# Performance work log

Hardware: AMD Instinct MI355X
Metric: run time of the kernel (lower is better)

## Reference

```python
import jax, jax.numpy as jnp
import numpy as np


def setup_inputs() -> dict:
    key = jax.random.key(0)
    k1, k2, k3 = jax.random.split(key, 3)
    inp = jax.random.normal(k1, (32, 128, 56, 56), dtype=jnp.float32)
    # kaiming-style scale for a 3x3 conv kernel
    fan_in = 128 * 3 * 3
    kernel = jax.random.normal(k2, (256, 128, 3, 3), dtype=jnp.float32) * np.float32(np.sqrt(2.0 / fan_in))
    bias = jax.random.normal(k3, (256,), dtype=jnp.float32)
    return {"inp": inp, "kernel": kernel, "bias": bias}


def reference(inp, kernel, bias):
    # 3x3 conv, stride 1, padding 1 (SAME), NCHW / OIHW layout, plus bias.
    out = jax.lax.conv_general_dilated(
        inp, kernel,
        window_strides=(1, 1),
        padding=((1, 1), (1, 1)),
        dimension_numbers=("NCHW", "OIHW", "NCHW"),
    )
    return out + bias[None, :, None, None]
```

## Files before the change

### kernel.cpp

```cpp
#include <hip/hip_runtime.h>
#include <hip/hip_bf16.h>


#define C_IN   128
#define K_OUT  256
#define HW     56
#define IMG    3136
#define NBATCH 32
#define PW     58
#define IN_WS_USHORT ((size_t)4*NBATCH*PW*256*8)
#define WT_WS_USHORT ((size_t)12*2*1536*8)

typedef __bf16 bf16x8 __attribute__((ext_vector_type(8)));
typedef float  f32x4  __attribute__((ext_vector_type(4)));
typedef unsigned short ushort8 __attribute__((ext_vector_type(8)));

__device__ inline unsigned short f2bf(float f) {
    unsigned int u = __builtin_bit_cast(unsigned int, f);
    u += ((u >> 16) & 1u) + 0x7FFFu;
    return (unsigned short)(u >> 16);
}

__device__ __forceinline__ void gl2lds16(const unsigned short* g, unsigned short* l) {
    __builtin_amdgcn_global_load_lds(
        (const __attribute__((address_space(1))) unsigned int*)g,
        (__attribute__((address_space(3))) unsigned int*)l, 16, 0, 0);
}

__global__ void prep_input(const float* __restrict__ inp,
                           unsigned short* __restrict__ dst) {
    __shared__ unsigned short tile[C_IN * 57];
    int n = blockIdx.x / PW, py = blockIdx.x % PW;
    ushort8* d8 = (ushort8*)dst;
    const bool border = (py == 0 || py == PW - 1);
    if (!border) {
        const float* src = inp + (size_t)n * C_IN * IMG + (py - 1) * HW;
        for (int i = threadIdx.x; i < C_IN * HW; i += 256) {
            int c = i / HW, x = i - c * HW;
            tile[c * 57 + x] = f2bf(src[c * IMG + x]);
        }
        __syncthreads();
    }
    for (int i = threadIdx.x; i < 1024; i += 256) {
        int cq = i >> 8, rem = i & 255;
        int X = ((rem >> 6) & 3) * 16 + (rem & 15);
        int cc = (rem >> 4) & 3;
        ushort8 v = (ushort8)0;
        if (!border && X >= 1 && X <= HW) {
#pragma unroll
            for (int e = 0; e < 8; ++e)
                v[e] = tile[(cq * 32 + cc * 8 + e) * 57 + (X - 1)];
        }
        d8[((size_t)(cq * NBATCH + n) * PW + py) * 256 + rem] = v;
    }
}

__global__ void prep_weights(const float* __restrict__ w,
                             unsigned short* __restrict__ dst) {
    int chunk = blockIdx.x * 256 + threadIdx.x;
    int p = chunk / 3072, rem = chunk - p * 3072;
    int koh = rem / 1536, rem2 = rem - koh * 1536;
    int s = rem2 / 512, rem3 = rem2 - s * 512;
    int koq = rem3 >> 6, cc = (rem3 >> 4) & 3, kor = rem3 & 15;
    int ko = koh * 128 + koq * 16 + kor;
    int cq = p / 3, r = p - 3 * cq;
    ushort8 v;
#pragma unroll
    for (int e = 0; e < 8; ++e)
        v[e] = f2bf(w[(ko * C_IN + cq * 32 + cc * 8 + e) * 9 + r * 3 + s]);
    ((ushort8*)dst)[chunk] = v;
}

__global__ __launch_bounds__(256, 2) void conv_mfma(
        const unsigned short* __restrict__ In,
        const unsigned short* __restrict__ Wt,
        const float* __restrict__ bias,
        float* __restrict__ out) {
    __shared__ unsigned short smem[16384];

    const int tid = threadIdx.x;
    const int lane = tid & 63, wv = tid >> 6;
    const int l15 = lane & 15, lk = lane >> 4;
    const int koh = blockIdx.y;
    const int by = blockIdx.x;
    const int n = by / 14, rb = (by % 14) * 4;

    const int wkol = (wv & 1) * 64;
    const int wpx  = (wv >> 1) * 112;
    const int wlane = (wv & 1) * 2048 + lk * 128 + l15 * 8;

    int yl[7], xp[3][7];
#pragma unroll
    for (int nf = 0; nf < 7; ++nf) {
        int p = wpx + nf * 16 + l15;
        yl[nf] = p / 56;
        int x = p - yl[nf] * 56;
#pragma unroll
        for (int s = 0; s < 3; ++s) {
            int X = x + s;
            xp[s][nf] = ((X >> 4) << 10) + lk * 256 + ((X & 15) << 4);
        }
    }

    f32x4 acc[4][7];
#pragma unroll
    for (int m = 0; m < 4; ++m)
#pragma unroll
        for (int nf = 0; nf < 7; ++nf) acc[m][nf] = (f32x4)0.0f;

    bf16x8 wbuf[2][4];

#define LOAD_WS(G_) do {                                                    \
    if constexpr ((G_) <= 35) {                                             \
        constexpr int p_ = (G_) / 3, sx_ = (G_) % 3;                        \
        const unsigned short* wp = Wt + ((size_t)(p_ * 2 + koh)) * 12288    \
                                   + sx_ * 4096 + wlane;                    \
        _Pragma("unroll")                                                   \
        for (int m = 0; m < 4; ++m)                                         \
            wbuf[(G_) & 1][m] = *(const bf16x8*)(wp + m * 512);             \
    } } while (0)

#define STAGE_ROW(C_, T_) do {                                              \
    gl2lds16(In + ((size_t)(((C_) * NBATCH + n) * PW + rb + (T_))) * 2048 + tid * 8, \
             &smem[((6 * (C_) + (T_)) & 7) * 2048 + tid * 8]);              \
} while (0)

#define STEP(PH, S_) do {                                                   \
    constexpr int g_ = (PH) * 3 + (S_);                                     \
    LOAD_WS(g_ + 1);                                                        \
    { const char* ib = (const char*)smem;                                   \
      bf16x8 b[7];                                                          \
      _Pragma("unroll")                                                     \
      for (int nf = 0; nf < 7; ++nf)                                        \
          b[nf] = *(const bf16x8*)(ib + roff[nf] + xp[(S_)][nf]);           \
      __builtin_amdgcn_s_setprio(1);                                        \
      _Pragma("unroll")                                                     \
      for (int m = 0; m < 4; ++m)                                           \
          _Pragma("unroll")                                                 \
          for (int nf = 0; nf < 7; ++nf)                                    \
              acc[m][nf] = __builtin_amdgcn_mfma_f32_16x16x32_bf16(         \
                  wbuf[g_ & 1][m], b[nf], acc[m][nf], 0, 0, 0);             \
      __builtin_amdgcn_s_setprio(0);                                        \
    }                                                                       \
} while (0)

    STAGE_ROW(0, 0); STAGE_ROW(0, 1); STAGE_ROW(0, 2); STAGE_ROW(0, 3);
    asm volatile("" ::: "memory");
    LOAD_WS(0);

#define PHASE(PH) do {                                                      \
    constexpr int cqp_ = (PH) / 3, rp_ = (PH) % 3;                          \
    asm volatile("s_waitcnt vmcnt(4)" ::: "memory");                        \
    asm volatile("s_barrier" ::: "memory");                                 \
    if constexpr (rp_ == 0) {                                               \
        STAGE_ROW(cqp_, 4);                                                 \
        if constexpr (cqp_ < 3) STAGE_ROW(cqp_ + 1, 0);                     \
    } else if constexpr (rp_ == 1) {                                        \
        STAGE_ROW(cqp_, 5);                                                 \
        if constexpr (cqp_ < 3) STAGE_ROW(cqp_ + 1, 1);                     \
    } else {                                                                \
        if constexpr (cqp_ < 3) { STAGE_ROW(cqp_ + 1, 2); STAGE_ROW(cqp_ + 1, 3); } \
    }                                                                       \
    { int roff[7];                                                          \
      _Pragma("unroll")                                                     \
      for (int nf = 0; nf < 7; ++nf)                                        \
          roff[nf] = ((6 * cqp_ + rp_ + yl[nf]) & 7) << 12;                 \
      STEP(PH, 0); STEP(PH, 1); STEP(PH, 2);                                \
    }                                                                       \
} while (0)

    PHASE(0);  PHASE(1);  PHASE(2);  PHASE(3);
    PHASE(4);  PHASE(5);  PHASE(6);  PHASE(7);
    PHASE(8);  PHASE(9);  PHASE(10); PHASE(11);

#undef PHASE
#undef STEP
#undef STAGE_ROW
#undef LOAD_WS

    const int sp0 = rb * 56 + wpx;
#pragma unroll
    for (int m = 0; m < 4; ++m) {
        int kb = koh * 128 + wkol + m * 16 + lk * 4;
        f32x4 bs = *(const f32x4*)(bias + kb);
#pragma unroll
        for (int nf = 0; nf < 7; ++nf) {
            float* ob = out + ((size_t)(n * K_OUT + kb) * IMG) + sp0 + nf * 16 + l15;
#pragma unroll
            for (int j = 0; j < 4; ++j)
                ob[(size_t)j * IMG] = acc[m][nf][j] + bs[j];
        }
    }
}

__global__ void conv_naive(const float* __restrict__ inp,
                           const float* __restrict__ ker,
                           const float* __restrict__ bias,
                           float* __restrict__ out, int total) {
    int o = blockIdx.x * blockDim.x + threadIdx.x;
    if (o >= total) return;
    int x = o % HW, y = (o / HW) % HW, ko = (o / IMG) % K_OUT, n = o / (IMG * K_OUT);
    float acc = bias[ko];
    for (int c = 0; c < C_IN; ++c)
        for (int r = 0; r < 3; ++r) {
            int iy = y + r - 1; if ((unsigned)iy >= HW) continue;
            for (int s = 0; s < 3; ++s) {
                int ix = x + s - 1; if ((unsigned)ix >= HW) continue;
                acc += inp[((n * C_IN + c) * HW + iy) * HW + ix]
                     * ker[((ko * C_IN + c) * 3 + r) * 3 + s];
            }
        }
    out[o] = acc;
}

extern "C" void kernel_launch(void* const* d_in, const int* in_sizes, int n_in,
                              void* d_out, int out_size, void* d_ws, size_t ws_size,
                              hipStream_t stream) {
    const float* inp  = (const float*)d_in[0];
    const float* ker  = (const float*)d_in[1];
    const float* bias = (const float*)d_in[2];
    float* out = (float*)d_out;

    const size_t need = (IN_WS_USHORT + WT_WS_USHORT) * 2;
    if (ws_size < need) {
        int total = NBATCH * K_OUT * IMG;
        conv_naive<<<(total + 255) / 256, 256, 0, stream>>>(inp, ker, bias, out, total);
        return;
    }

    unsigned short* inb = (unsigned short*)d_ws;
    unsigned short* wtb = inb + IN_WS_USHORT;

    prep_input<<<NBATCH * PW, 256, 0, stream>>>(inp, inb);
    prep_weights<<<144, 256, 0, stream>>>(ker, wtb);

    conv_mfma<<<dim3(448, 2), 256, 0, stream>>>(inb, wtb, bias, out);
}
```

Baseline: 98.69 us.

## Replace 8-row LDS ring with double-buffered 6-row tiles per channel quarter

Input staging changes from a rolling 8-row LDS ring, refilled two rows per phase across 12 phases, to a double buffer holding 6 rows for each of the 4 channel quarters. Each phase prefetches the whole next quarter and then runs all 9 filter taps. This cuts the s_waitcnt plus barrier synchronisation points from 12 to 4 and simplifies the row-offset arithmetic, since the modulo-8 wrap is gone. In exchange, LDS use per block grows from 32 KB to 48 KB, which could limit occupancy, and prefetches are issued in larger, coarser batches.

```diff
diff --git a/kernel.cpp b/kernel.cpp
--- a/kernel.cpp
+++ b/kernel.cpp
@@ -76,7 +76,7 @@
         const unsigned short* __restrict__ Wt,
         const float* __restrict__ bias,
         float* __restrict__ out) {
-    __shared__ unsigned short smem[16384];
+    __shared__ unsigned short smem[24576];
 
     const int tid = threadIdx.x;
     const int lane = tid & 63, wv = tid >> 6;
@@ -120,16 +120,18 @@
             wbuf[(G_) & 1][m] = *(const bf16x8*)(wp + m * 512);             \
     } } while (0)
 
-#define STAGE_ROW(C_, T_) do {                                              \
-    gl2lds16(In + ((size_t)(((C_) * NBATCH + n) * PW + rb + (T_))) * 2048 + tid * 8, \
-             &smem[((6 * (C_) + (T_)) & 7) * 2048 + tid * 8]);              \
-} while (0)
-
-#define STEP(PH, S_) do {                                                   \
-    constexpr int g_ = (PH) * 3 + (S_);                                     \
+#define STAGE6(CQN) do {                                                    \
+    _Pragma("unroll")                                                       \
+    for (int t = 0; t < 6; ++t)                                             \
+        gl2lds16(In + ((size_t)(((CQN) * NBATCH + n) * PW + rb + t)) * 2048 + tid * 8, \
+                 &smem[(((CQN) & 1) * 6 + t) * 2048 + tid * 8]);            \
+    asm volatile("" ::: "memory");    \
+} while (0)
+
+#define STEP(CQ_, R_, S_) do {                                              \
+    constexpr int g_ = (CQ_) * 9 + (R_) * 3 + (S_);                         \
     LOAD_WS(g_ + 1);                                                        \
-    { const char* ib = (const char*)smem;                                   \
-      bf16x8 b[7];                                                          \
+    { bf16x8 b[7];                                                          \
       _Pragma("unroll")                                                     \
       for (int nf = 0; nf < 7; ++nf)                                        \
           b[nf] = *(const bf16x8*)(ib + roff[nf] + xp[(S_)][nf]);           \
@@ -144,38 +146,33 @@
     }                                                                       \
 } while (0)
 
-    STAGE_ROW(0, 0); STAGE_ROW(0, 1); STAGE_ROW(0, 2); STAGE_ROW(0, 3);
-    asm volatile("" ::: "memory");
+#define ROFF(CQ_, R_) do {                                                  \
+    _Pragma("unroll")                                                       \
+    for (int nf = 0; nf < 7; ++nf)                                          \
+        roff[nf] = (((CQ_) & 1) * 6 + (R_) + yl[nf]) << 12;                 \
+} while (0)
+
+    STAGE6(0);
     LOAD_WS(0);
 
-#define PHASE(PH) do {                                                      \
-    constexpr int cqp_ = (PH) / 3, rp_ = (PH) % 3;                          \
+#define PHASE(CQ_) do {                                                     \
     asm volatile("s_waitcnt vmcnt(4)" ::: "memory");                        \
     asm volatile("s_barrier" ::: "memory");                                 \
-    if constexpr (rp_ == 0) {                                               \
-        STAGE_ROW(cqp_, 4);                                                 \
-        if constexpr (cqp_ < 3) STAGE_ROW(cqp_ + 1, 0);                     \
-    } else if constexpr (rp_ == 1) {                                        \
-        STAGE_ROW(cqp_, 5);                                                 \
-        if constexpr (cqp_ < 3) STAGE_ROW(cqp_ + 1, 1);                     \
-    } else {                                                                \
-        if constexpr (cqp_ < 3) { STAGE_ROW(cqp_ + 1, 2); STAGE_ROW(cqp_ + 1, 3); } \
+    if constexpr ((CQ_) < 3) STAGE6((CQ_) + 1);                             \
+    { const char* ib = (const char*)smem;                                   \
+      int roff[7];                                                          \
+      ROFF(CQ_, 0); STEP(CQ_,0,0); STEP(CQ_,0,1); STEP(CQ_,0,2);            \
+      ROFF(CQ_, 1); STEP(CQ_,1,0); STEP(CQ_,1,1); STEP(CQ_,1,2);            \
+      ROFF(CQ_, 2); STEP(CQ_,2,0); STEP(CQ_,2,1); STEP(CQ_,2,2);            \
     }                                                                       \
-    { int roff[7];                                                          \
-      _Pragma("unroll")                                                     \
-      for (int nf = 0; nf < 7; ++nf)                                        \
-          roff[nf] = ((6 * cqp_ + rp_ + yl[nf]) & 7) << 12;                 \
-      STEP(PH, 0); STEP(PH, 1); STEP(PH, 2);                                \
-    }                                                                       \
 } while (0)
 
     PHASE(0);  PHASE(1);  PHASE(2);  PHASE(3);
-    PHASE(4);  PHASE(5);  PHASE(6);  PHASE(7);
-    PHASE(8);  PHASE(9);  PHASE(10); PHASE(11);
 
 #undef PHASE
+#undef ROFF
 #undef STEP
-#undef STAGE_ROW
+#undef STAGE6
 #undef LOAD_WS
 
     const int sp0 = rb * 56 + wpx;
```

After: 81.55 us. 17.4% less time.
